# Kernel optimization log

Measured on AMD Instinct MI355X. Metric: run time of the kernel, lower is better.

## Reference

```python
import jax, jax.numpy as jnp
import numpy as np

RMS_EPS = 1e-6


def setup_inputs() -> dict:
    key = jax.random.key(0)
    ks = jax.random.split(key, 6)
    B, S, D, F, E = 4, 2048, 1024, 4096, 8
    scale = 0.02
    return {
        "hidden_states": jax.random.normal(ks[0], (B, S, D), dtype=jnp.float32),
        "norm_weight": jnp.ones((D,), dtype=jnp.float32),
        "gate_w": jax.random.normal(ks[1], (E, D), dtype=jnp.float32) * scale,
        "w1": jax.random.normal(ks[2], (E, D, F), dtype=jnp.float32) * scale,
        "w3": jax.random.normal(ks[3], (E, D, F), dtype=jnp.float32) * scale,
        "w2": jax.random.normal(ks[4], (E, F, D), dtype=jnp.float32) * scale,
        "top_k": 2,
    }


def reference(hidden_states, norm_weight, gate_w, w1, w3, w2, top_k):
    B, S, D = hidden_states.shape
    E = gate_w.shape[0]
    # norm_fn: RMSNorm (pre-MoE norm in Mixtral block)
    x = hidden_states * jax.lax.rsqrt(jnp.mean(jnp.square(hidden_states), axis=-1, keepdims=True) + RMS_EPS)
    x = (x * norm_weight).reshape(-1, D)  # [T, D], T = B*S
    # router
    router_logits = jnp.einsum('td,ed->te', x, gate_w)  # [T, E]
    routing = jax.nn.softmax(router_logits.astype(jnp.float32), axis=-1)
    top_w, top_idx = jax.lax.top_k(routing, top_k)  # [T, k]
    top_w = top_w / jnp.sum(top_w, axis=-1, keepdims=True)
    top_w = top_w.astype(x.dtype)
    # dense-masked expert combine: tokens not routed to expert e get weight 0,
    # mathematically identical to the gather/scatter loop in the original.
    out = jnp.zeros_like(x)
    for e in range(E):  # fixed small loop over experts
        w_e = jnp.sum(jnp.where(top_idx == e, top_w, 0.0), axis=-1)  # [T]
        h = jax.nn.silu(x @ w1[e]) * (x @ w3[e])  # [T, F] SwiGLU expert
        out = out + w_e[:, None] * (h @ w2[e])
    return out.reshape(B, S, D), router_logits
```

## Files before the change

kernel.cpp:

```cpp
#include <hip/hip_runtime.h>
#include <hip/hip_bf16.h>

#define T_TOK 8192
#define D_DIM 1024
#define F_DIM 4096
#define E_NUM 8

typedef short s16x8 __attribute__((ext_vector_type(8)));
typedef float f32x4 __attribute__((ext_vector_type(4)));
typedef unsigned short u16x8 __attribute__((ext_vector_type(8)));

__device__ __forceinline__ unsigned short f2bf(float f) {
  union { float f; unsigned int u; } v; v.f = f;
  unsigned int u = v.u;
  return (unsigned short)((u + 0x7FFFu + ((u >> 16) & 1u)) >> 16);
}

__device__ __forceinline__ void async16(const void* g, void* l) {
  __builtin_amdgcn_global_load_lds((const __attribute__((address_space(1))) void*)g,
                                   (__attribute__((address_space(3))) void*)l, 16, 0, 0);
}

__global__ __launch_bounds__(256) void norm_router_kernel(
    const float* __restrict__ hs, const float* __restrict__ nw,
    const float* __restrict__ gw, unsigned short* __restrict__ xb,
    float* __restrict__ logits_out, int* __restrict__ cnt,
    int* __restrict__ ilist, float* __restrict__ wlist) {
  int t = blockIdx.x;
  int tid = threadIdx.x;
  int lane = tid & 63, wid = tid >> 6;
  float4 v = ((const float4*)(hs + (size_t)t * D_DIM))[tid];
  float ss = v.x * v.x + v.y * v.y + v.z * v.z + v.w * v.w;
#pragma unroll
  for (int o = 32; o > 0; o >>= 1) ss += __shfl_xor(ss, o);
  __shared__ float red[4];
  __shared__ float pl[4][8];
  if (lane == 0) red[wid] = ss;
  __syncthreads();
  float ms = (red[0] + red[1] + red[2] + red[3]) * (1.0f / 1024.0f);
  float rs = rsqrtf(ms + 1e-6f);
  float4 wv = ((const float4*)nw)[tid];
  float x0 = v.x * rs * wv.x, x1 = v.y * rs * wv.y;
  float x2 = v.z * rs * wv.z, x3 = v.w * rs * wv.w;
  ((ushort4*)(xb + (size_t)t * D_DIM))[tid] =
      make_ushort4(f2bf(x0), f2bf(x1), f2bf(x2), f2bf(x3));
  float p[8];
#pragma unroll
  for (int e = 0; e < 8; ++e) {
    float4 g = ((const float4*)(gw + (size_t)e * D_DIM))[tid];
    p[e] = x0 * g.x + x1 * g.y + x2 * g.z + x3 * g.w;
  }
#pragma unroll
  for (int e = 0; e < 8; ++e) {
#pragma unroll
    for (int o = 32; o > 0; o >>= 1) p[e] += __shfl_xor(p[e], o);
  }
  if (lane == 0) {
#pragma unroll
    for (int e = 0; e < 8; ++e) pl[wid][e] = p[e];
  }
  __syncthreads();
  if (tid == 0) {
    float l[8];
#pragma unroll
    for (int e = 0; e < 8; ++e) {
      l[e] = pl[0][e] + pl[1][e] + pl[2][e] + pl[3][e];
      logits_out[(size_t)t * 8 + e] = l[e];
    }
    int i0 = 0; float b0 = l[0];
#pragma unroll
    for (int e = 1; e < 8; ++e) if (l[e] > b0) { b0 = l[e]; i0 = e; }
    int i1 = (i0 == 0) ? 1 : 0; float b1 = l[i1];
#pragma unroll
    for (int e = 0; e < 8; ++e) if (e != i0 && l[e] > b1) { b1 = l[e]; i1 = e; }
    float wa = 1.0f / (1.0f + __expf(b1 - b0));
    float wb = 1.0f / (1.0f + __expf(b0 - b1));
    int p0 = atomicAdd(&cnt[i0], 1);
    ilist[i0 * T_TOK + p0] = t * 2;     wlist[i0 * T_TOK + p0] = wa;
    int p1 = atomicAdd(&cnt[i1], 1);
    ilist[i1 * T_TOK + p1] = t * 2 + 1; wlist[i1 * T_TOK + p1] = wb;
  }
}

__global__ __launch_bounds__(256) void transpose_cvt_kernel(
    const float* __restrict__ w1, const float* __restrict__ w3,
    const float* __restrict__ w2, unsigned short* __restrict__ w13t,
    unsigned short* __restrict__ w2t) {
  __shared__ unsigned short tileS[64][72];
  int bx = blockIdx.x;
  int tensor = bx >> 13;
  int e = (bx >> 10) & 7;
  int tl = bx & 1023;
  const float* src; int C, tr, tc;
  if (tensor == 0) {
    src = w1 + (size_t)e * D_DIM * F_DIM; C = F_DIM; tr = tl >> 6; tc = tl & 63;
  } else if (tensor == 1) {
    src = w3 + (size_t)e * D_DIM * F_DIM; C = F_DIM; tr = tl >> 6; tc = tl & 63;
  } else {
    src = w2 + (size_t)e * F_DIM * D_DIM; C = D_DIM; tr = tl >> 4; tc = tl & 15;
  }
  int r0 = tr * 64, c0 = tc * 64;
  int tid = threadIdx.x;
  int rr = tid >> 4, ccb = (tid & 15) * 4;
#pragma unroll
  for (int i = 0; i < 4; ++i) {
    int r = rr + i * 16;
    float4 v = *(const float4*)(src + (size_t)(r0 + r) * C + c0 + ccb);
    tileS[ccb + 0][r] = f2bf(v.x);
    tileS[ccb + 1][r] = f2bf(v.y);
    tileS[ccb + 2][r] = f2bf(v.z);
    tileS[ccb + 3][r] = f2bf(v.w);
  }
  __syncthreads();
  int row = tid >> 2, col = (tid & 3) * 16;
  unsigned short* dp;
  if (tensor < 2) {
    int f = c0 + row;
    int prow = ((f >> 6) * 128) + (f & 63) + (tensor == 1 ? 64 : 0);
    dp = w13t + ((size_t)e * 8192 + prow) * D_DIM + r0 + col;
  } else {
    dp = w2t + ((size_t)e * D_DIM + c0 + row) * F_DIM + r0 + col;
  }
  u16x8 v0, v1;
#pragma unroll
  for (int j = 0; j < 8; ++j) { v0[j] = tileS[row][col + j]; v1[j] = tileS[row][col + 8 + j]; }
  *(u16x8*)dp = v0;
  *(u16x8*)(dp + 8) = v1;
}

__global__ __launch_bounds__(256, 2) void gemm1_kernel(
    const unsigned short* __restrict__ xb, const unsigned short* __restrict__ w13t,
    unsigned short* __restrict__ H, const int* __restrict__ cnt,
    const int* __restrict__ ilist) {
  int flat = blockIdx.x;
  int e = flat & 7;
  int work = flat >> 3;
  int rt = work & 63;
  int ft = work >> 6;
  int ne = cnt[e];
  int r0 = rt * 128;
  if (r0 >= ne) return;
  __shared__ __align__(16) unsigned short As[3 * 4096];
  __shared__ __align__(16) unsigned short Bs[3 * 8192];
  __shared__ int toks[128];
  int tid = threadIdx.x, lane = tid & 63, w = tid >> 6;
  if (tid < 128) toks[tid] = ilist[e * T_TOK + min(r0 + tid, ne - 1)];
  __syncthreads();
  const unsigned short* bpanel = w13t + ((size_t)e * 8192 + ft * 256) * D_DIM;
  int la = lane >> 2, lc4 = lane & 3;
  int ra0 = w * 32 + la, ra1 = ra0 + 16;
  const unsigned short* ap0 = xb + (size_t)(toks[ra0] >> 1) * D_DIM + ((lc4 ^ ((ra0 >> 1) & 3)) * 8);
  const unsigned short* ap1 = xb + (size_t)(toks[ra1] >> 1) * D_DIM + ((lc4 ^ ((ra1 >> 1) & 3)) * 8);
  int da0 = ra0 * 32 + lc4 * 8;
  int da1 = ra1 * 32 + lc4 * 8;
  int rb0 = w * 64 + la, rb1 = rb0 + 16, rb2 = rb0 + 32, rb3 = rb0 + 48;
  const unsigned short* bp0 = bpanel + (size_t)rb0 * D_DIM + ((lc4 ^ ((rb0 >> 1) & 3)) * 8);
  const unsigned short* bp1 = bpanel + (size_t)rb1 * D_DIM + ((lc4 ^ ((rb1 >> 1) & 3)) * 8);
  const unsigned short* bp2 = bpanel + (size_t)rb2 * D_DIM + ((lc4 ^ ((rb2 >> 1) & 3)) * 8);
  const unsigned short* bp3 = bpanel + (size_t)rb3 * D_DIM + ((lc4 ^ ((rb3 >> 1) & 3)) * 8);
  int db0 = rb0 * 32 + lc4 * 8, db1 = rb1 * 32 + lc4 * 8;
  int db2 = rb2 * 32 + lc4 * 8, db3 = rb3 * 32 + lc4 * 8;
  int wr = w >> 1, wc = w & 1;
  int lr = lane & 15, lc = lane >> 4;
  int aoff[4], boff[8];
#pragma unroll
  for (int m = 0; m < 4; ++m) {
    int row = wr * 64 + m * 16 + lr;
    aoff[m] = row * 32 + ((lc ^ ((row >> 1) & 3)) * 8);
  }
#pragma unroll
  for (int n = 0; n < 8; ++n) {
    int row = wc * 128 + n * 16 + lr;
    boff[n] = row * 32 + ((lc ^ ((row >> 1) & 3)) * 8);
  }
  f32x4 acc[4][8] = {};
  async16(ap0, &As[da0]); async16(ap1, &As[da1]);
  async16(bp0, &Bs[db0]); async16(bp1, &Bs[db1]);
  async16(bp2, &Bs[db2]); async16(bp3, &Bs[db3]);
  async16(ap0 + 32, &As[4096 + da0]); async16(ap1 + 32, &As[4096 + da1]);
  async16(bp0 + 32, &Bs[8192 + db0]); async16(bp1 + 32, &Bs[8192 + db1]);
  async16(bp2 + 32, &Bs[8192 + db2]); async16(bp3 + 32, &Bs[8192 + db3]);

#define G1_STEP(T_, BUF_, VMC_, DOST_)                                          \
  {                                                                             \
    asm volatile("s_waitcnt vmcnt(" VMC_ ")" ::: "memory");                     \
    __builtin_amdgcn_s_barrier();                                               \
    if (DOST_) {                                                                \
      int nk = ((T_) + 2) * 32;                                                 \
      async16(ap0 + nk, &As[(((BUF_) + 2) % 3) * 4096 + da0]);                  \
      async16(ap1 + nk, &As[(((BUF_) + 2) % 3) * 4096 + da1]);                  \
      async16(bp0 + nk, &Bs[(((BUF_) + 2) % 3) * 8192 + db0]);                  \
      async16(bp1 + nk, &Bs[(((BUF_) + 2) % 3) * 8192 + db1]);                  \
      async16(bp2 + nk, &Bs[(((BUF_) + 2) % 3) * 8192 + db2]);                  \
      async16(bp3 + nk, &Bs[(((BUF_) + 2) % 3) * 8192 + db3]);                  \
    }                                                                           \
    {                                                                           \
      const unsigned short* Ab = &As[(BUF_) * 4096];                            \
      const unsigned short* Bb = &Bs[(BUF_) * 8192];                            \
      s16x8 a[4], b[8];                                                         \
      _Pragma("unroll") for (int m = 0; m < 4; ++m)                             \
          a[m] = *(const s16x8*)(Ab + aoff[m]);                                 \
      _Pragma("unroll") for (int n = 0; n < 8; ++n)                             \
          b[n] = *(const s16x8*)(Bb + boff[n]);                                 \
      _Pragma("unroll") for (int m = 0; m < 4; ++m)                             \
          _Pragma("unroll") for (int n = 0; n < 8; ++n)                         \
              acc[m][n] = __builtin_amdgcn_mfma_f32_16x16x32_bf16(              \
                  a[m], b[n], acc[m][n], 0, 0, 0);                              \
    }                                                                           \
  }

  for (int tb = 0; tb < 30; tb += 3) {
    G1_STEP(tb, 0, "6", 1)
    G1_STEP(tb + 1, 1, "6", 1)
    G1_STEP(tb + 2, 2, "6", 1)
  }
  G1_STEP(30, 0, "6", 0)
  G1_STEP(31, 1, "0", 0)
#undef G1_STEP

  int g4 = lane >> 4, cl = lane & 15;
  int fbase = (2 * ft + wc) * 64;
#pragma unroll
  for (int m = 0; m < 4; ++m) {
#pragma unroll
    for (int j = 0; j < 4; ++j) {
      int rloc = wr * 64 + m * 16 + g4 * 4 + j;
      if (r0 + rloc < ne) {
        unsigned short* hp = H + (size_t)toks[rloc] * F_DIM + fbase + cl;
#pragma unroll
        for (int n = 0; n < 4; ++n) {
          float c1 = acc[m][n][j], c3 = acc[m][n + 4][j];
          float h = c1 / (1.0f + __expf(-c1)) * c3;
          hp[n * 16] = f2bf(h);
        }
      }
    }
  }
}

__global__ __launch_bounds__(256, 2) void gemm2_kernel(
    const unsigned short* __restrict__ H, const unsigned short* __restrict__ w2t,
    const int* __restrict__ cnt, const int* __restrict__ ilist,
    const float* __restrict__ wlist, float* __restrict__ out) {
  int flat = blockIdx.x;
  int e = flat & 7;
  int work = flat >> 3;
  int rt = work & 63;
  int n0i = work >> 6;
  int ne = cnt[e];
  int r0 = rt * 128;
  if (r0 >= ne) return;
  int n0 = n0i * 256;
  __shared__ __align__(16) unsigned short As[3 * 4096];
  __shared__ __align__(16) unsigned short Bs[3 * 8192];
  __shared__ int toks[128];
  __shared__ float wts[128];
  int tid = threadIdx.x, lane = tid & 63, w = tid >> 6;
  if (tid < 128) {
    int idx = e * T_TOK + min(r0 + tid, ne - 1);
    toks[tid] = ilist[idx];
    wts[tid] = wlist[idx];
  }
  __syncthreads();
  const unsigned short* bpanel = w2t + ((size_t)e * D_DIM + n0) * F_DIM;
  int la = lane >> 2, lc4 = lane & 3;
  int ra0 = w * 32 + la, ra1 = ra0 + 16;
  const unsigned short* ap0 = H + (size_t)toks[ra0] * F_DIM + ((lc4 ^ ((ra0 >> 1) & 3)) * 8);
  const unsigned short* ap1 = H + (size_t)toks[ra1] * F_DIM + ((lc4 ^ ((ra1 >> 1) & 3)) * 8);
  int da0 = ra0 * 32 + lc4 * 8;
  int da1 = ra1 * 32 + lc4 * 8;
  int rb0 = w * 64 + la, rb1 = rb0 + 16, rb2 = rb0 + 32, rb3 = rb0 + 48;
  const unsigned short* bp0 = bpanel + (size_t)rb0 * F_DIM + ((lc4 ^ ((rb0 >> 1) & 3)) * 8);
  const unsigned short* bp1 = bpanel + (size_t)rb1 * F_DIM + ((lc4 ^ ((rb1 >> 1) & 3)) * 8);
  const unsigned short* bp2 = bpanel + (size_t)rb2 * F_DIM + ((lc4 ^ ((rb2 >> 1) & 3)) * 8);
  const unsigned short* bp3 = bpanel + (size_t)rb3 * F_DIM + ((lc4 ^ ((rb3 >> 1) & 3)) * 8);
  int db0 = rb0 * 32 + lc4 * 8, db1 = rb1 * 32 + lc4 * 8;
  int db2 = rb2 * 32 + lc4 * 8, db3 = rb3 * 32 + lc4 * 8;
  int wr = w >> 1, wc = w & 1;
  int lr = lane & 15, lc = lane >> 4;
  int aoff[4], boff[8];
#pragma unroll
  for (int m = 0; m < 4; ++m) {
    int row = wr * 64 + m * 16 + lr;
    aoff[m] = row * 32 + ((lc ^ ((row >> 1) & 3)) * 8);
  }
#pragma unroll
  for (int n = 0; n < 8; ++n) {
    int row = wc * 128 + n * 16 + lr;
    boff[n] = row * 32 + ((lc ^ ((row >> 1) & 3)) * 8);
  }
  f32x4 acc[4][8] = {};
  async16(ap0, &As[da0]); async16(ap1, &As[da1]);
  async16(bp0, &Bs[db0]); async16(bp1, &Bs[db1]);
  async16(bp2, &Bs[db2]); async16(bp3, &Bs[db3]);
  async16(ap0 + 32, &As[4096 + da0]); async16(ap1 + 32, &As[4096 + da1]);
  async16(bp0 + 32, &Bs[8192 + db0]); async16(bp1 + 32, &Bs[8192 + db1]);
  async16(bp2 + 32, &Bs[8192 + db2]); async16(bp3 + 32, &Bs[8192 + db3]);

#define G2_STEP(T_, BUF_, VMC_, DOST_)                                          \
  {                                                                             \
    asm volatile("s_waitcnt vmcnt(" VMC_ ")" ::: "memory");                     \
    __builtin_amdgcn_s_barrier();                                               \
    if (DOST_) {                                                                \
      int nk = ((T_) + 2) * 32;                                                 \
      async16(ap0 + nk, &As[(((BUF_) + 2) % 3) * 4096 + da0]);                  \
      async16(ap1 + nk, &As[(((BUF_) + 2) % 3) * 4096 + da1]);                  \
      async16(bp0 + nk, &Bs[(((BUF_) + 2) % 3) * 8192 + db0]);                  \
      async16(bp1 + nk, &Bs[(((BUF_) + 2) % 3) * 8192 + db1]);                  \
      async16(bp2 + nk, &Bs[(((BUF_) + 2) % 3) * 8192 + db2]);                  \
      async16(bp3 + nk, &Bs[(((BUF_) + 2) % 3) * 8192 + db3]);                  \
    }                                                                           \
    {                                                                           \
      const unsigned short* Ab = &As[(BUF_) * 4096];                            \
      const unsigned short* Bb = &Bs[(BUF_) * 8192];                            \
      s16x8 a[4], b[8];                                                         \
      _Pragma("unroll") for (int m = 0; m < 4; ++m)                             \
          a[m] = *(const s16x8*)(Ab + aoff[m]);                                 \
      _Pragma("unroll") for (int n = 0; n < 8; ++n)                             \
          b[n] = *(const s16x8*)(Bb + boff[n]);                                 \
      _Pragma("unroll") for (int m = 0; m < 4; ++m)                             \
          _Pragma("unroll") for (int n = 0; n < 8; ++n)                         \
              acc[m][n] = __builtin_amdgcn_mfma_f32_16x16x32_bf16(              \
                  a[m], b[n], acc[m][n], 0, 0, 0);                              \
    }                                                                           \
  }

  for (int tb = 0; tb < 126; tb += 3) {
    G2_STEP(tb, 0, "6", 1)
    G2_STEP(tb + 1, 1, "6", 1)
    G2_STEP(tb + 2, 2, "6", 1)
  }
  G2_STEP(126, 0, "6", 0)
  G2_STEP(127, 1, "0", 0)
#undef G2_STEP

  int g4 = lane >> 4, cl = lane & 15;
#pragma unroll
  for (int m = 0; m < 4; ++m) {
#pragma unroll
    for (int j = 0; j < 4; ++j) {
      int rloc = wr * 64 + m * 16 + g4 * 4 + j;
      if (r0 + rloc < ne) {
        int tok = toks[rloc] >> 1;
        float ww = wts[rloc];
        float* op = out + (size_t)tok * D_DIM + n0 + wc * 128 + cl;
#pragma unroll
        for (int n = 0; n < 8; ++n)
          unsafeAtomicAdd(op + n * 16, ww * acc[m][n][j]);
      }
    }
  }
}

extern "C" void kernel_launch(void* const* d_in, const int* in_sizes, int n_in,
                              void* d_out, int out_size, void* d_ws, size_t ws_size,
                              hipStream_t stream) {
  const float* hs = (const float*)d_in[0];
  const float* nw = (const float*)d_in[1];
  const float* gw = (const float*)d_in[2];
  const float* w1 = (const float*)d_in[3];
  const float* w3 = (const float*)d_in[4];
  const float* w2 = (const float*)d_in[5];
  float* out = (float*)d_out;
  float* logits_out = out + (size_t)T_TOK * D_DIM;

  char* ws = (char*)d_ws;
  unsigned short* xb   = (unsigned short*)(ws);
  unsigned short* w13t = (unsigned short*)(ws + 16777216ull);
  unsigned short* w2t  = (unsigned short*)(ws + 150994944ull);
  unsigned short* H    = (unsigned short*)(ws + 218103808ull);
  int*   ilist = (int*)(ws + 352321536ull);
  float* wlist = (float*)(ws + 352583680ull);
  int*   cnt   = (int*)(ws + 352845824ull);

  hipMemsetAsync(d_out, 0, (size_t)out_size * sizeof(float), stream);
  hipMemsetAsync(cnt, 0, E_NUM * sizeof(int), stream);
  norm_router_kernel<<<T_TOK, 256, 0, stream>>>(hs, nw, gw, xb, logits_out, cnt, ilist, wlist);
  transpose_cvt_kernel<<<3 * E_NUM * 1024, 256, 0, stream>>>(w1, w3, w2, w13t, w2t);
  gemm1_kernel<<<E_NUM * 64 * 32, 256, 0, stream>>>(xb, w13t, H, cnt, ilist);
  gemm2_kernel<<<E_NUM * 64 * 4, 256, 0, stream>>>(H, w2t, cnt, ilist, wlist, out);
}
```

Before: 975.8 us.

## Enlarge MoE GEMM tiles to 256x256 with 512 threads and interleaved loads

Both expert GEMMs move from 128x256 tiles on 256 threads to 256x256 tiles on 512 threads (8 waves in a 2x4 grid). This halves the number of passes over the weight panels per token tile and raises arithmetic intensity. The w1/w3 interleave in the transposed weight layout changes from 64-row to 32-row groups so each wave's columns still pair gate and up projections. Inside each k-step the B-tile prefetch is split from the A prefetch and placed between two MFMA halves, with s_setprio raised around the MFMA blocks. The trade-off is more LDS (96KB) and more accumulator registers per thread, which may lower occupancy, plus coarser work granularity for experts with few tokens.

```diff
diff --git a/kernel.cpp b/kernel.cpp
--- a/kernel.cpp
+++ b/kernel.cpp
@@ -116,7 +116,7 @@
   unsigned short* dp;
   if (tensor < 2) {
     int f = c0 + row;
-    int prow = ((f >> 6) * 128) + (f & 63) + (tensor == 1 ? 64 : 0);
+    int prow = ((f >> 5) * 64) + (f & 31) + (tensor == 1 ? 32 : 0);
     dp = w13t + ((size_t)e * 8192 + prow) * D_DIM + r0 + col;
   } else {
     dp = w2t + ((size_t)e * D_DIM + c0 + row) * F_DIM + r0 + col;
@@ -128,108 +128,111 @@
   *(u16x8*)(dp + 8) = v1;
 }
 
-__global__ __launch_bounds__(256, 2) void gemm1_kernel(
+__global__ __launch_bounds__(512, 2) void gemm1_kernel(
     const unsigned short* __restrict__ xb, const unsigned short* __restrict__ w13t,
     unsigned short* __restrict__ H, const int* __restrict__ cnt,
     const int* __restrict__ ilist) {
   int flat = blockIdx.x;
   int e = flat & 7;
   int work = flat >> 3;
-  int rt = work & 63;
-  int ft = work >> 6;
+  int rt = work & 31;
+  int ft = work >> 5;
   int ne = cnt[e];
-  int r0 = rt * 128;
+  int r0 = rt * 256;
   if (r0 >= ne) return;
-  __shared__ __align__(16) unsigned short As[3 * 4096];
+  __shared__ __align__(16) unsigned short As[3 * 8192];
   __shared__ __align__(16) unsigned short Bs[3 * 8192];
-  __shared__ int toks[128];
+  __shared__ int toks[256];
   int tid = threadIdx.x, lane = tid & 63, w = tid >> 6;
-  if (tid < 128) toks[tid] = ilist[e * T_TOK + min(r0 + tid, ne - 1)];
+  if (tid < 256) toks[tid] = ilist[e * T_TOK + min(r0 + tid, ne - 1)];
   __syncthreads();
   const unsigned short* bpanel = w13t + ((size_t)e * 8192 + ft * 256) * D_DIM;
-  int la = lane >> 2, lc4 = lane & 3;
-  int ra0 = w * 32 + la, ra1 = ra0 + 16;
-  const unsigned short* ap0 = xb + (size_t)(toks[ra0] >> 1) * D_DIM + ((lc4 ^ ((ra0 >> 1) & 3)) * 8);
-  const unsigned short* ap1 = xb + (size_t)(toks[ra1] >> 1) * D_DIM + ((lc4 ^ ((ra1 >> 1) & 3)) * 8);
-  int da0 = ra0 * 32 + lc4 * 8;
-  int da1 = ra1 * 32 + lc4 * 8;
-  int rb0 = w * 64 + la, rb1 = rb0 + 16, rb2 = rb0 + 32, rb3 = rb0 + 48;
-  const unsigned short* bp0 = bpanel + (size_t)rb0 * D_DIM + ((lc4 ^ ((rb0 >> 1) & 3)) * 8);
-  const unsigned short* bp1 = bpanel + (size_t)rb1 * D_DIM + ((lc4 ^ ((rb1 >> 1) & 3)) * 8);
-  const unsigned short* bp2 = bpanel + (size_t)rb2 * D_DIM + ((lc4 ^ ((rb2 >> 1) & 3)) * 8);
-  const unsigned short* bp3 = bpanel + (size_t)rb3 * D_DIM + ((lc4 ^ ((rb3 >> 1) & 3)) * 8);
-  int db0 = rb0 * 32 + lc4 * 8, db1 = rb1 * 32 + lc4 * 8;
-  int db2 = rb2 * 32 + lc4 * 8, db3 = rb3 * 32 + lc4 * 8;
-  int wr = w >> 1, wc = w & 1;
+  int sr0 = tid >> 2, sr1 = sr0 + 128;
+  int ch0 = (((tid & 3) ^ ((sr0 >> 1) & 3)) * 8);
+  int ch1 = (((tid & 3) ^ ((sr1 >> 1) & 3)) * 8);
+  const unsigned short* ap0 = xb + (size_t)(toks[sr0] >> 1) * D_DIM + ch0;
+  const unsigned short* ap1 = xb + (size_t)(toks[sr1] >> 1) * D_DIM + ch1;
+  const unsigned short* bp0 = bpanel + (size_t)sr0 * D_DIM + ch0;
+  const unsigned short* bp1 = bpanel + (size_t)sr1 * D_DIM + ch1;
+  int d0 = (sr0 * 32) + (tid & 3) * 8;
+  int d1 = d0 + 4096;
+  int wr = w >> 2, wc = w & 3;
   int lr = lane & 15, lc = lane >> 4;
-  int aoff[4], boff[8];
-#pragma unroll
-  for (int m = 0; m < 4; ++m) {
-    int row = wr * 64 + m * 16 + lr;
+  int aoff[8], boff[4];
+#pragma unroll
+  for (int m = 0; m < 8; ++m) {
+    int row = wr * 128 + m * 16 + lr;
     aoff[m] = row * 32 + ((lc ^ ((row >> 1) & 3)) * 8);
   }
 #pragma unroll
-  for (int n = 0; n < 8; ++n) {
-    int row = wc * 128 + n * 16 + lr;
+  for (int n = 0; n < 4; ++n) {
+    int row = wc * 64 + n * 16 + lr;
     boff[n] = row * 32 + ((lc ^ ((row >> 1) & 3)) * 8);
   }
-  f32x4 acc[4][8] = {};
-  async16(ap0, &As[da0]); async16(ap1, &As[da1]);
-  async16(bp0, &Bs[db0]); async16(bp1, &Bs[db1]);
-  async16(bp2, &Bs[db2]); async16(bp3, &Bs[db3]);
-  async16(ap0 + 32, &As[4096 + da0]); async16(ap1 + 32, &As[4096 + da1]);
-  async16(bp0 + 32, &Bs[8192 + db0]); async16(bp1 + 32, &Bs[8192 + db1]);
-  async16(bp2 + 32, &Bs[8192 + db2]); async16(bp3 + 32, &Bs[8192 + db3]);
+  f32x4 acc[8][4] = {};
+  async16(ap0, &As[d0]); async16(ap1, &As[d1]);
+  async16(bp0, &Bs[d0]); async16(bp1, &Bs[d1]);
+  async16(ap0 + 32, &As[8192 + d0]); async16(ap1 + 32, &As[8192 + d1]);
+  async16(bp0 + 32, &Bs[8192 + d0]); async16(bp1 + 32, &Bs[8192 + d1]);
 
 #define G1_STEP(T_, BUF_, VMC_, DOST_)                                          \
   {                                                                             \
     asm volatile("s_waitcnt vmcnt(" VMC_ ")" ::: "memory");                     \
     __builtin_amdgcn_s_barrier();                                               \
-    if (DOST_) {                                                                \
+    const unsigned short* Ab = &As[(BUF_) * 8192];                              \
+    const unsigned short* Bb = &Bs[(BUF_) * 8192];                              \
+    s16x8 a[8], b[4];                                                           \
+    if (DOST_) {                                   \
       int nk = ((T_) + 2) * 32;                                                 \
-      async16(ap0 + nk, &As[(((BUF_) + 2) % 3) * 4096 + da0]);                  \
-      async16(ap1 + nk, &As[(((BUF_) + 2) % 3) * 4096 + da1]);                  \
-      async16(bp0 + nk, &Bs[(((BUF_) + 2) % 3) * 8192 + db0]);                  \
-      async16(bp1 + nk, &Bs[(((BUF_) + 2) % 3) * 8192 + db1]);                  \
-      async16(bp2 + nk, &Bs[(((BUF_) + 2) % 3) * 8192 + db2]);                  \
-      async16(bp3 + nk, &Bs[(((BUF_) + 2) % 3) * 8192 + db3]);                  \
+      async16(ap0 + nk, &As[(((BUF_) + 2) % 3) * 8192 + d0]);                   \
+      async16(ap1 + nk, &As[(((BUF_) + 2) % 3) * 8192 + d1]);                   \
     }                                                                           \
-    {                                                                           \
-      const unsigned short* Ab = &As[(BUF_) * 4096];                            \
-      const unsigned short* Bb = &Bs[(BUF_) * 8192];                            \
-      s16x8 a[4], b[8];                                                         \
-      _Pragma("unroll") for (int m = 0; m < 4; ++m)                             \
-          a[m] = *(const s16x8*)(Ab + aoff[m]);                                 \
-      _Pragma("unroll") for (int n = 0; n < 8; ++n)                             \
-          b[n] = *(const s16x8*)(Bb + boff[n]);                                 \
-      _Pragma("unroll") for (int m = 0; m < 4; ++m)                             \
-          _Pragma("unroll") for (int n = 0; n < 8; ++n)                         \
-              acc[m][n] = __builtin_amdgcn_mfma_f32_16x16x32_bf16(              \
-                  a[m], b[n], acc[m][n], 0, 0, 0);                              \
+    _Pragma("unroll") for (int m = 0; m < 4; ++m)                               \
+        a[m] = *(const s16x8*)(Ab + aoff[m]);                                   \
+    _Pragma("unroll") for (int n = 0; n < 4; ++n)                               \
+        b[n] = *(const s16x8*)(Bb + boff[n]);                                   \
+    __builtin_amdgcn_s_setprio(1);                                              \
+    _Pragma("unroll") for (int m = 0; m < 4; ++m)                               \
+        _Pragma("unroll") for (int n = 0; n < 4; ++n)                           \
+            acc[m][n] = __builtin_amdgcn_mfma_f32_16x16x32_bf16(                \
+                a[m], b[n], acc[m][n], 0, 0, 0);                                \
+    __builtin_amdgcn_s_setprio(0);                                              \
+    if (DOST_) {                                   \
+      int nk = ((T_) + 2) * 32;                                                 \
+      async16(bp0 + nk, &Bs[(((BUF_) + 2) % 3) * 8192 + d0]);                   \
+      async16(bp1 + nk, &Bs[(((BUF_) + 2) % 3) * 8192 + d1]);                   \
     }                                                                           \
+    _Pragma("unroll") for (int m = 4; m < 8; ++m)                               \
+        a[m] = *(const s16x8*)(Ab + aoff[m]);                                   \
+    __builtin_amdgcn_s_setprio(1);                                              \
+    _Pragma("unroll") for (int m = 4; m < 8; ++m)                               \
+        _Pragma("unroll") for (int n = 0; n < 4; ++n)                           \
+            acc[m][n] = __builtin_amdgcn_mfma_f32_16x16x32_bf16(                \
+                a[m], b[n], acc[m][n], 0, 0, 0);                                \
+    __builtin_amdgcn_s_setprio(0);                                              \
   }
 
   for (int tb = 0; tb < 30; tb += 3) {
-    G1_STEP(tb, 0, "6", 1)
-    G1_STEP(tb + 1, 1, "6", 1)
-    G1_STEP(tb + 2, 2, "6", 1)
-  }
-  G1_STEP(30, 0, "6", 0)
+    G1_STEP(tb, 0, "4", 1)
+    G1_STEP(tb + 1, 1, "4", 1)
+    G1_STEP(tb + 2, 2, "4", 1)
+  }
+  G1_STEP(30, 0, "4", 0)
   G1_STEP(31, 1, "0", 0)
 #undef G1_STEP
 
   int g4 = lane >> 4, cl = lane & 15;
-  int fbase = (2 * ft + wc) * 64;
-#pragma unroll
-  for (int m = 0; m < 4; ++m) {
+  int fbase = (4 * ft + wc) * 32;
+#pragma unroll
+  for (int m = 0; m < 8; ++m) {
 #pragma unroll
     for (int j = 0; j < 4; ++j) {
-      int rloc = wr * 64 + m * 16 + g4 * 4 + j;
+      int rloc = wr * 128 + m * 16 + g4 * 4 + j;
       if (r0 + rloc < ne) {
         unsigned short* hp = H + (size_t)toks[rloc] * F_DIM + fbase + cl;
 #pragma unroll
-        for (int n = 0; n < 4; ++n) {
-          float c1 = acc[m][n][j], c3 = acc[m][n + 4][j];
+        for (int n = 0; n < 2; ++n) {
+          float c1 = acc[m][n][j], c3 = acc[m][n + 2][j];
           float h = c1 / (1.0f + __expf(-c1)) * c3;
           hp[n * 16] = f2bf(h);
         }
@@ -238,114 +241,116 @@
   }
 }
 
-__global__ __launch_bounds__(256, 2) void gemm2_kernel(
+__global__ __launch_bounds__(512, 2) void gemm2_kernel(
     const unsigned short* __restrict__ H, const unsigned short* __restrict__ w2t,
     const int* __restrict__ cnt, const int* __restrict__ ilist,
     const float* __restrict__ wlist, float* __restrict__ out) {
   int flat = blockIdx.x;
   int e = flat & 7;
   int work = flat >> 3;
-  int rt = work & 63;
-  int n0i = work >> 6;
+  int rt = work & 31;
+  int nt = work >> 5;
   int ne = cnt[e];
-  int r0 = rt * 128;
+  int r0 = rt * 256;
   if (r0 >= ne) return;
-  int n0 = n0i * 256;
-  __shared__ __align__(16) unsigned short As[3 * 4096];
+  __shared__ __align__(16) unsigned short As[3 * 8192];
   __shared__ __align__(16) unsigned short Bs[3 * 8192];
-  __shared__ int toks[128];
-  __shared__ float wts[128];
+  __shared__ int toks[256];
+  __shared__ float wts[256];
   int tid = threadIdx.x, lane = tid & 63, w = tid >> 6;
-  if (tid < 128) {
+  if (tid < 256) {
     int idx = e * T_TOK + min(r0 + tid, ne - 1);
     toks[tid] = ilist[idx];
     wts[tid] = wlist[idx];
   }
   __syncthreads();
-  const unsigned short* bpanel = w2t + ((size_t)e * D_DIM + n0) * F_DIM;
-  int la = lane >> 2, lc4 = lane & 3;
-  int ra0 = w * 32 + la, ra1 = ra0 + 16;
-  const unsigned short* ap0 = H + (size_t)toks[ra0] * F_DIM + ((lc4 ^ ((ra0 >> 1) & 3)) * 8);
-  const unsigned short* ap1 = H + (size_t)toks[ra1] * F_DIM + ((lc4 ^ ((ra1 >> 1) & 3)) * 8);
-  int da0 = ra0 * 32 + lc4 * 8;
-  int da1 = ra1 * 32 + lc4 * 8;
-  int rb0 = w * 64 + la, rb1 = rb0 + 16, rb2 = rb0 + 32, rb3 = rb0 + 48;
-  const unsigned short* bp0 = bpanel + (size_t)rb0 * F_DIM + ((lc4 ^ ((rb0 >> 1) & 3)) * 8);
-  const unsigned short* bp1 = bpanel + (size_t)rb1 * F_DIM + ((lc4 ^ ((rb1 >> 1) & 3)) * 8);
-  const unsigned short* bp2 = bpanel + (size_t)rb2 * F_DIM + ((lc4 ^ ((rb2 >> 1) & 3)) * 8);
-  const unsigned short* bp3 = bpanel + (size_t)rb3 * F_DIM + ((lc4 ^ ((rb3 >> 1) & 3)) * 8);
-  int db0 = rb0 * 32 + lc4 * 8, db1 = rb1 * 32 + lc4 * 8;
-  int db2 = rb2 * 32 + lc4 * 8, db3 = rb3 * 32 + lc4 * 8;
-  int wr = w >> 1, wc = w & 1;
+  const unsigned short* bpanel = w2t + ((size_t)e * D_DIM + nt * 256) * F_DIM;
+  int sr0 = tid >> 2, sr1 = sr0 + 128;
+  int ch0 = (((tid & 3) ^ ((sr0 >> 1) & 3)) * 8);
+  int ch1 = (((tid & 3) ^ ((sr1 >> 1) & 3)) * 8);
+  const unsigned short* ap0 = H + (size_t)toks[sr0] * F_DIM + ch0;
+  const unsigned short* ap1 = H + (size_t)toks[sr1] * F_DIM + ch1;
+  const unsigned short* bp0 = bpanel + (size_t)sr0 * F_DIM + ch0;
+  const unsigned short* bp1 = bpanel + (size_t)sr1 * F_DIM + ch1;
+  int d0 = (sr0 * 32) + (tid & 3) * 8;
+  int d1 = d0 + 4096;
+  int wr = w >> 2, wc = w & 3;
   int lr = lane & 15, lc = lane >> 4;
-  int aoff[4], boff[8];
-#pragma unroll
-  for (int m = 0; m < 4; ++m) {
-    int row = wr * 64 + m * 16 + lr;
+  int aoff[8], boff[4];
+#pragma unroll
+  for (int m = 0; m < 8; ++m) {
+    int row = wr * 128 + m * 16 + lr;
     aoff[m] = row * 32 + ((lc ^ ((row >> 1) & 3)) * 8);
   }
 #pragma unroll
-  for (int n = 0; n < 8; ++n) {
-    int row = wc * 128 + n * 16 + lr;
+  for (int n = 0; n < 4; ++n) {
+    int row = wc * 64 + n * 16 + lr;
     boff[n] = row * 32 + ((lc ^ ((row >> 1) & 3)) * 8);
   }
-  f32x4 acc[4][8] = {};
-  async16(ap0, &As[da0]); async16(ap1, &As[da1]);
-  async16(bp0, &Bs[db0]); async16(bp1, &Bs[db1]);
-  async16(bp2, &Bs[db2]); async16(bp3, &Bs[db3]);
-  async16(ap0 + 32, &As[4096 + da0]); async16(ap1 + 32, &As[4096 + da1]);
-  async16(bp0 + 32, &Bs[8192 + db0]); async16(bp1 + 32, &Bs[8192 + db1]);
-  async16(bp2 + 32, &Bs[8192 + db2]); async16(bp3 + 32, &Bs[8192 + db3]);
+  f32x4 acc[8][4] = {};
+  async16(ap0, &As[d0]); async16(ap1, &As[d1]);
+  async16(bp0, &Bs[d0]); async16(bp1, &Bs[d1]);
+  async16(ap0 + 32, &As[8192 + d0]); async16(ap1 + 32, &As[8192 + d1]);
+  async16(bp0 + 32, &Bs[8192 + d0]); async16(bp1 + 32, &Bs[8192 + d1]);
 
 #define G2_STEP(T_, BUF_, VMC_, DOST_)                                          \
   {                                                                             \
     asm volatile("s_waitcnt vmcnt(" VMC_ ")" ::: "memory");                     \
     __builtin_amdgcn_s_barrier();                                               \
+    const unsigned short* Ab = &As[(BUF_) * 8192];                              \
+    const unsigned short* Bb = &Bs[(BUF_) * 8192];                              \
+    s16x8 a[8], b[4];                                                           \
     if (DOST_) {                                                                \
       int nk = ((T_) + 2) * 32;                                                 \
-      async16(ap0 + nk, &As[(((BUF_) + 2) % 3) * 4096 + da0]);                  \
-      async16(ap1 + nk, &As[(((BUF_) + 2) % 3) * 4096 + da1]);                  \
-      async16(bp0 + nk, &Bs[(((BUF_) + 2) % 3) * 8192 + db0]);                  \
-      async16(bp1 + nk, &Bs[(((BUF_) + 2) % 3) * 8192 + db1]);                  \
-      async16(bp2 + nk, &Bs[(((BUF_) + 2) % 3) * 8192 + db2]);                  \
-      async16(bp3 + nk, &Bs[(((BUF_) + 2) % 3) * 8192 + db3]);                  \
+      async16(ap0 + nk, &As[(((BUF_) + 2) % 3) * 8192 + d0]);                   \
+      async16(ap1 + nk, &As[(((BUF_) + 2) % 3) * 8192 + d1]);                   \
     }                                                                           \
-    {                                                                           \
-      const unsigned short* Ab = &As[(BUF_) * 4096];                            \
-      const unsigned short* Bb = &Bs[(BUF_) * 8192];                            \
-      s16x8 a[4], b[8];                                                         \
-      _Pragma("unroll") for (int m = 0; m < 4; ++m)                             \
-          a[m] = *(const s16x8*)(Ab + aoff[m]);                                 \
-      _Pragma("unroll") for (int n = 0; n < 8; ++n)                             \
-          b[n] = *(const s16x8*)(Bb + boff[n]);                                 \
-      _Pragma("unroll") for (int m = 0; m < 4; ++m)                             \
-          _Pragma("unroll") for (int n = 0; n < 8; ++n)                         \
-              acc[m][n] = __builtin_amdgcn_mfma_f32_16x16x32_bf16(              \
-                  a[m], b[n], acc[m][n], 0, 0, 0);                              \
+    _Pragma("unroll") for (int m = 0; m < 4; ++m)                               \
+        a[m] = *(const s16x8*)(Ab + aoff[m]);                                   \
+    _Pragma("unroll") for (int n = 0; n < 4; ++n)                               \
+        b[n] = *(const s16x8*)(Bb + boff[n]);                                   \
+    __builtin_amdgcn_s_setprio(1);                                              \
+    _Pragma("unroll") for (int m = 0; m < 4; ++m)                               \
+        _Pragma("unroll") for (int n = 0; n < 4; ++n)                           \
+            acc[m][n] = __builtin_amdgcn_mfma_f32_16x16x32_bf16(                \
+                a[m], b[n], acc[m][n], 0, 0, 0);                                \
+    __builtin_amdgcn_s_setprio(0);                                              \
+    if (DOST_) {                                                                \
+      int nk = ((T_) + 2) * 32;                                                 \
+      async16(bp0 + nk, &Bs[(((BUF_) + 2) % 3) * 8192 + d0]);                   \
+      async16(bp1 + nk, &Bs[(((BUF_) + 2) % 3) * 8192 + d1]);                   \
     }                                                                           \
+    _Pragma("unroll") for (int m = 4; m < 8; ++m)                               \
+        a[m] = *(const s16x8*)(Ab + aoff[m]);                                   \
+    __builtin_amdgcn_s_setprio(1);                                              \
+    _Pragma("unroll") for (int m = 4; m < 8; ++m)                               \
+        _Pragma("unroll") for (int n = 0; n < 4; ++n)                           \
+            acc[m][n] = __builtin_amdgcn_mfma_f32_16x16x32_bf16(                \
+                a[m], b[n], acc[m][n], 0, 0, 0);                                \
+    __builtin_amdgcn_s_setprio(0);                                              \
   }
 
   for (int tb = 0; tb < 126; tb += 3) {
-    G2_STEP(tb, 0, "6", 1)
-    G2_STEP(tb + 1, 1, "6", 1)
-    G2_STEP(tb + 2, 2, "6", 1)
-  }
-  G2_STEP(126, 0, "6", 0)
+    G2_STEP(tb, 0, "4", 1)
+    G2_STEP(tb + 1, 1, "4", 1)
+    G2_STEP(tb + 2, 2, "4", 1)
+  }
+  G2_STEP(126, 0, "4", 0)
   G2_STEP(127, 1, "0", 0)
 #undef G2_STEP
 
   int g4 = lane >> 4, cl = lane & 15;
 #pragma unroll
-  for (int m = 0; m < 4; ++m) {
+  for (int m = 0; m < 8; ++m) {
 #pragma unroll
     for (int j = 0; j < 4; ++j) {
-      int rloc = wr * 64 + m * 16 + g4 * 4 + j;
+      int rloc = wr * 128 + m * 16 + g4 * 4 + j;
       if (r0 + rloc < ne) {
         int tok = toks[rloc] >> 1;
         float ww = wts[rloc];
-        float* op = out + (size_t)tok * D_DIM + n0 + wc * 128 + cl;
-#pragma unroll
-        for (int n = 0; n < 8; ++n)
+        float* op = out + (size_t)tok * D_DIM + nt * 256 + wc * 64 + cl;
+#pragma unroll
+        for (int n = 0; n < 4; ++n)
           unsafeAtomicAdd(op + n * 16, ww * acc[m][n][j]);
       }
     }
@@ -377,6 +382,6 @@
   hipMemsetAsync(cnt, 0, E_NUM * sizeof(int), stream);
   norm_router_kernel<<<T_TOK, 256, 0, stream>>>(hs, nw, gw, xb, logits_out, cnt, ilist, wlist);
   transpose_cvt_kernel<<<3 * E_NUM * 1024, 256, 0, stream>>>(w1, w3, w2, w13t, w2t);
-  gemm1_kernel<<<E_NUM * 64 * 32, 256, 0, stream>>>(xb, w13t, H, cnt, ilist);
-  gemm2_kernel<<<E_NUM * 64 * 4, 256, 0, stream>>>(H, w2t, cnt, ilist, wlist, out);
-}
+  gemm1_kernel<<<E_NUM * 32 * 32, 512, 0, stream>>>(xb, w13t, H, cnt, ilist);
+  gemm2_kernel<<<E_NUM * 32 * 4, 512, 0, stream>>>(H, w2t, cnt, ilist, wlist, out);
+}
```

After: 923.6 us. 1.06x faster.
